# Kernel tuning notes

Measured on AMD Instinct MI355X. Metric: run time of the kernel, lower is better.

## Reference

```python
import jax, jax.numpy as jnp
import numpy as np

N_NODES = 100000
N_EDGES = 1600000
IN_CH = 165
HID = 128


def _xavier(key, shape):
    fan_out, fan_in = shape
    lim = float(np.sqrt(6.0 / (fan_in + fan_out)))
    return jax.random.uniform(key, shape, jnp.float32, -lim, lim)


def setup_inputs() -> dict:
    key = jax.random.key(0)
    ks = jax.random.split(key, 8)
    x = jax.random.normal(ks[0], (N_NODES, IN_CH), jnp.float32)
    edge_index = jax.random.randint(ks[1], (2, N_EDGES), 0, N_NODES, jnp.int64)
    return {
        "x": x,
        "edge_index": edge_index,
        "W_l0": _xavier(ks[2], (HID, IN_CH)),
        "b_l0": jnp.zeros((HID,), jnp.float32),
        "W_r0": _xavier(ks[3], (HID, IN_CH)),
        "W_l1": _xavier(ks[4], (HID, HID)),
        "b_l1": jnp.zeros((HID,), jnp.float32),
        "W_r1": _xavier(ks[5], (HID, HID)),
        "W_l2": _xavier(ks[6], (HID, HID)),
        "b_l2": jnp.zeros((HID,), jnp.float32),
        "W_r2": _xavier(ks[7], (HID, HID)),
        "W_out": _xavier(jax.random.fold_in(key, 7), (2, HID)),
        "b_out": jnp.zeros((2,), jnp.float32),
    }


def _sage_conv(x, src, dst, W_l, b_l, W_r):
    # mean-aggregate source features into destination nodes
    msg = x[src]  # [E, d] gather
    agg = jax.ops.segment_sum(msg, dst, num_segments=N_NODES)  # [N, d]
    cnt = jax.ops.segment_sum(jnp.ones((src.shape[0], 1), x.dtype), dst,
                              num_segments=N_NODES)
    mean = agg / jnp.maximum(cnt, 1.0)
    # out = lin_l(mean) + lin_r(x); lin_r has no bias (PyG SAGEConv)
    return mean @ W_l.T + b_l + x @ W_r.T


def reference(x, edge_index, W_l0, b_l0, W_r0, W_l1, b_l1, W_r1,
              W_l2, b_l2, W_r2, W_out, b_out):
    src, dst = edge_index[0], edge_index[1]
    h = jax.nn.relu(_sage_conv(x, src, dst, W_l0, b_l0, W_r0))
    h = jax.nn.relu(_sage_conv(h, src, dst, W_l1, b_l1, W_r1))
    h = _sage_conv(h, src, dst, W_l2, b_l2, W_r2)
    # dropout is identity in inference
    return h @ W_out.T + b_out  # [N, 2]
```

## Files before the change

### kernel.cpp

```cpp
#include <hip/hip_runtime.h>
#include <cstdint>
#include <cstddef>

#define NN 100000
#define IN_CH 165
#define HID 128

#define NBUCK 196
#define NPB 512
#define BMAX 10240
#define NWG 256

typedef __attribute__((ext_vector_type(8))) short short8;
typedef __attribute__((ext_vector_type(4))) float f32x4;

__device__ __forceinline__ ushort f2bf(float v) {
    uint b = __builtin_bit_cast(uint, v);
    return (ushort)((b + 0x7FFFu + ((b >> 16) & 1u)) >> 16);
}
__device__ __forceinline__ float lo16f(uint u) { return __builtin_bit_cast(float, u << 16); }
__device__ __forceinline__ float hi16f(uint u) { return __builtin_bit_cast(float, u & 0xFFFF0000u); }

__global__ __launch_bounds__(256) void k_cnt(const int* __restrict__ dst, int E, int chunk,
                                             int* __restrict__ cnt) {
    __shared__ int h[NBUCK];
    const int w = blockIdx.x, t = threadIdx.x;
    for (int b = t; b < NBUCK; b += 256) h[b] = 0;
    __syncthreads();
    const int beg = w * chunk, end = min(E, beg + chunk);
    for (int i0 = beg + t * 8; i0 < end; i0 += 2048) {
        if (i0 + 8 <= end) {
            const int4 d0 = *reinterpret_cast<const int4*>(dst + i0);
            const int4 d1 = *reinterpret_cast<const int4*>(dst + i0 + 4);
            atomicAdd(&h[d0.x >> 9], 1);
            atomicAdd(&h[d0.y >> 9], 1);
            atomicAdd(&h[d0.z >> 9], 1);
            atomicAdd(&h[d0.w >> 9], 1);
            atomicAdd(&h[d1.x >> 9], 1);
            atomicAdd(&h[d1.y >> 9], 1);
            atomicAdd(&h[d1.z >> 9], 1);
            atomicAdd(&h[d1.w >> 9], 1);
        } else {
            for (int i = i0; i < end; ++i) atomicAdd(&h[dst[i] >> 9], 1);
        }
    }
    __syncthreads();
    for (int b = t; b < NBUCK; b += 256) cnt[b * NWG + w] = h[b];
}

__global__ __launch_bounds__(1024) void k_cscan(const int* __restrict__ cnt,
                                                int* __restrict__ gaddr) {
    __shared__ int ps[1024];
    const int t = threadIdx.x;
    int s = 0;
    for (int k = 0; k < 49; k++) s += cnt[t * 49 + k];
    ps[t] = s;
    __syncthreads();
    for (int off = 1; off < 1024; off <<= 1) {
        int v = (t >= off) ? ps[t - off] : 0;
        __syncthreads();
        ps[t] += v;
        __syncthreads();
    }
    int run = (t > 0) ? ps[t - 1] : 0;
    for (int k = 0; k < 49; k++) {
        const int m = t * 49 + k;
        gaddr[m] = run;
        run += cnt[m];
    }
}

__global__ __launch_bounds__(256) void k_scatter(const int* __restrict__ src,
                                                 const int* __restrict__ dst, int E, int chunk,
                                                 const int* __restrict__ gaddr,
                                                 int* __restrict__ bdata) {
    __shared__ int cur[NBUCK];
    __shared__ int thist[256];
    __shared__ int sA[256];
    __shared__ int tex[NBUCK];
    __shared__ int lpos[NBUCK];
    __shared__ int staged[2048];
    __shared__ int addrs[2048];
    const int w = blockIdx.x, t = threadIdx.x;
    for (int b = t; b < NBUCK; b += 256) cur[b] = gaddr[b * NWG + w];
    const int beg = w * chunk, end = min(E, beg + chunk);
    for (int tb = beg; tb < end; tb += 2048) {
        const int tcnt = min(2048, end - tb);
        int key[8], bk[8];
        const int i0 = tb + t * 8;
        if (i0 + 8 <= end) {
            const int4 d0 = *reinterpret_cast<const int4*>(dst + i0);
            const int4 d1 = *reinterpret_cast<const int4*>(dst + i0 + 4);
            const int4 s0 = *reinterpret_cast<const int4*>(src + i0);
            const int4 s1 = *reinterpret_cast<const int4*>(src + i0 + 4);
            bk[0] = d0.x >> 9; key[0] = (s0.x << 9) | (d0.x & 511);
            bk[1] = d0.y >> 9; key[1] = (s0.y << 9) | (d0.y & 511);
            bk[2] = d0.z >> 9; key[2] = (s0.z << 9) | (d0.z & 511);
            bk[3] = d0.w >> 9; key[3] = (s0.w << 9) | (d0.w & 511);
            bk[4] = d1.x >> 9; key[4] = (s1.x << 9) | (d1.x & 511);
            bk[5] = d1.y >> 9; key[5] = (s1.y << 9) | (d1.y & 511);
            bk[6] = d1.z >> 9; key[6] = (s1.z << 9) | (d1.z & 511);
            bk[7] = d1.w >> 9; key[7] = (s1.w << 9) | (d1.w & 511);
        } else {
#pragma unroll
            for (int j = 0; j < 8; j++) {
                const int i = i0 + j;
                if (i < end) {
                    const int d = dst[i];
                    bk[j] = d >> 9;
                    key[j] = (src[i] << 9) | (d & 511);
                } else bk[j] = -1;
            }
        }
        __syncthreads();
        thist[t] = 0;
        __syncthreads();
#pragma unroll
        for (int j = 0; j < 8; j++)
            if (bk[j] >= 0) atomicAdd(&thist[bk[j]], 1);
        __syncthreads();
        sA[t] = thist[t];
        __syncthreads();
        for (int off = 1; off < 256; off <<= 1) {
            int v = (t >= off) ? sA[t - off] : 0;
            __syncthreads();
            sA[t] += v;
            __syncthreads();
        }
        if (t < NBUCK) {
            const int e = sA[t] - thist[t];
            tex[t] = e;
            lpos[t] = e;
        }
        __syncthreads();
#pragma unroll
        for (int j = 0; j < 8; j++)
            if (bk[j] >= 0) {
                const int b = bk[j];
                const int l = atomicAdd(&lpos[b], 1);
                staged[l] = key[j];
                addrs[l] = cur[b] + (l - tex[b]);
            }
        __syncthreads();
        for (int l = t; l < tcnt; l += 256) bdata[addrs[l]] = staged[l];
        __syncthreads();
        if (t < NBUCK) cur[t] += thist[t];
    }
}

__global__ __launch_bounds__(256) void k_csr2(const int* __restrict__ gaddr,
                                              const int* __restrict__ bdata, int E,
                                              int* __restrict__ csr, int* __restrict__ row_off,
                                              float* __restrict__ inv, int N) {
    __shared__ int keys[BMAX];
    __shared__ int sorted[BMAX];
    __shared__ int h5[NPB];
    __shared__ int s5[NPB];
    const int b = blockIdx.x, t = threadIdx.x;
    const int base = gaddr[b * NWG];
    const int nxt = (b == NBUCK - 1) ? E : gaddr[(b + 1) * NWG];
    const int tot = min(nxt - base, BMAX);
    for (int i = t; i < tot; i += 256) keys[i] = bdata[base + i];
    h5[t] = 0;
    h5[t + 256] = 0;
    __syncthreads();
    for (int i = t; i < tot; i += 256) atomicAdd(&h5[keys[i] & 511], 1);
    __syncthreads();
    s5[t] = h5[t];
    s5[t + 256] = h5[t + 256];
    __syncthreads();
    for (int off = 1; off < 512; off <<= 1) {
        const int a = (t >= off) ? s5[t - off] : 0;
        const int c = (t + 256 >= off) ? s5[t + 256 - off] : 0;
        __syncthreads();
        s5[t] += a;
        s5[t + 256] += c;
        __syncthreads();
    }
    const int e0 = s5[t] - h5[t];
    const int e1 = s5[t + 256] - h5[t + 256];
    __syncthreads();
    s5[t] = e0;
    s5[t + 256] = e1;
    const int n0 = b * NPB + t, n1 = b * NPB + t + 256;
    if (n0 < N) { row_off[n0] = base + e0; inv[n0] = 1.0f / (float)max(h5[t], 1); }
    if (n1 < N) { row_off[n1] = base + e1; inv[n1] = 1.0f / (float)max(h5[t + 256], 1); }
    if (b == 0 && t == 0) row_off[N] = E;
    __syncthreads();
    for (int i = t; i < tot; i += 256) {
        const int k = keys[i];
        const int p = atomicAdd(&s5[k & 511], 1);
        sorted[p] = k;
    }
    __syncthreads();
    for (int i = t; i < tot; i += 256) csr[base + i] = sorted[i] >> 9;
}

__device__ __forceinline__ void wpack_one(const float* __restrict__ W, int K, int idx,
                                          ushort* __restrict__ Wh) {
    const int k = idx >> 7;
    const int j = idx & 127;
    const float v = (k < K) ? W[j * K + k] : 0.0f;
    const int o = (k >> 3) * (HID * 8) + j * 8 + (k & 7);
    Wh[o] = f2bf(v);
}

__global__ __launch_bounds__(256) void k_prep(
    const float* __restrict__ Wl0, const float* __restrict__ Wr0,
    const float* __restrict__ Wl1, const float* __restrict__ Wr1,
    const float* __restrict__ Wl2, const float* __restrict__ Wr2,
    const float* __restrict__ Wout, const float* __restrict__ bl2,
    const float* __restrict__ bout,
    ushort* __restrict__ Wl0h, ushort* __restrict__ Wr0h,
    ushort* __restrict__ Wl1h, ushort* __restrict__ Wr1h,
    float* __restrict__ Wzp, float* __restrict__ bz)
{
    if (blockIdx.x == 96) {
        const int t = threadIdx.x;
        const int c = t >> 7, k = t & 127;
        float sl = 0.f, sr = 0.f;
        for (int j = 0; j < 128; j++) {
            const float wo = Wout[c * 128 + j];
            sl += wo * Wl2[j * 128 + k];
            sr += wo * Wr2[j * 128 + k];
        }
        Wzp[c * 128 + k] = sl;
        Wzp[256 + c * 128 + k] = sr;
        if (t < 2) {
            float s = bout[t];
            for (int j = 0; j < 128; j++) s += Wout[t * 128 + j] * bl2[j];
            bz[t] = s;
        }
        return;
    }
    const int gid = blockIdx.x * 256 + threadIdx.x;
    if (gid < 192 * HID) {
        wpack_one(Wl0, IN_CH, gid, Wl0h);
        wpack_one(Wr0, IN_CH, gid, Wr0h);
    }
    if (gid < 128 * HID) {
        wpack_one(Wl1, HID, gid, Wl1h);
        wpack_one(Wr1, HID, gid, Wr1h);
    }
}

template <typename TIN, int K, int KP>
__global__ __launch_bounds__(256) void k_gemm_mfma(
    const TIN* __restrict__ h,
    const ushort* __restrict__ Wlh, const ushort* __restrict__ Wrh,
    ushort* __restrict__ yl, ushort* __restrict__ yr)
{
    constexpr int RS = KP * 2;
    __shared__ __align__(16) char Ah[32 * RS];
    const int tid = threadIdx.x;
    const int node0 = blockIdx.x * 32;
    const TIN* __restrict__ hp = h + (size_t)node0 * K;

    if constexpr (sizeof(TIN) == 2) {
        constexpr int Q = 32 * (KP / 8);
        for (int q = tid; q < Q; q += 256) {
            const int r = q / (KP / 8);
            const int kp = (q - r * (KP / 8)) * 8;
            const short8 v = *reinterpret_cast<const short8*>(&hp[r * K + kp]);
            const int byte = r * RS + ((kp * 2) ^ ((r & 7) << 4));
            *reinterpret_cast<short8*>(Ah + byte) = v;
        }
    } else {
        __shared__ __align__(16) float raw[32 * K];
        const float* __restrict__ hpf = (const float*)hp;
        for (int i = tid * 4; i < 32 * K; i += 1024)
            *reinterpret_cast<float4*>(&raw[i]) = *reinterpret_cast<const float4*>(&hpf[i]);
        __syncthreads();
        constexpr int G = KP / 4;
        for (int q = tid; q < 32 * G; q += 256) {
            const int r = q / G;
            const int kp = (q - r * G) * 4;
            const float v0 = (kp + 0 < K) ? raw[r * K + kp + 0] : 0.0f;
            const float v1 = (kp + 1 < K) ? raw[r * K + kp + 1] : 0.0f;
            const float v2 = (kp + 2 < K) ? raw[r * K + kp + 2] : 0.0f;
            const float v3 = (kp + 3 < K) ? raw[r * K + kp + 3] : 0.0f;
            const int byte = r * RS + ((kp * 2) ^ ((r & 7) << 4));
            *reinterpret_cast<ushort4*>(Ah + byte) =
                make_ushort4(f2bf(v0), f2bf(v1), f2bf(v2), f2bf(v3));
        }
    }
    __syncthreads();

    const int lane = tid & 63;
    const int w = tid >> 6;
    const int trow = lane & 15;
    const int kg = lane >> 4;
    const ushort* __restrict__ Bh = (w & 1) ? Wrh : Wlh;
    ushort* __restrict__ yo = (w & 1) ? yr : yl;
    const int cb0 = (w >> 1) * 4;

    f32x4 acc[2][4];
#pragma unroll
    for (int a = 0; a < 2; ++a)
#pragma unroll
        for (int b = 0; b < 4; ++b) acc[a][b] = (f32x4){0.f, 0.f, 0.f, 0.f};

    const int xo = (trow & 7) << 4;
    const char* __restrict__ pA0 = Ah + trow * RS;
    const char* __restrict__ pA1 = Ah + (trow + 16) * RS;

    constexpr int KS = KP / 32;
    for (int ks = 0; ks < KS; ++ks) {
        const int kbyte = (ks * 64 + kg * 16) ^ xo;
        const short8 a0h = *reinterpret_cast<const short8*>(pA0 + kbyte);
        const short8 a1h = *reinterpret_cast<const short8*>(pA1 + kbyte);
        const int bbase = (ks * 4 + kg) * (HID * 8) + trow * 8;
#pragma unroll
        for (int ci = 0; ci < 4; ++ci) {
            const short8 bh = *reinterpret_cast<const short8*>(Bh + bbase + (cb0 + ci) * 128);
            acc[0][ci] = __builtin_amdgcn_mfma_f32_16x16x32_bf16(a0h, bh, acc[0][ci], 0, 0, 0);
            acc[1][ci] = __builtin_amdgcn_mfma_f32_16x16x32_bf16(a1h, bh, acc[1][ci], 0, 0, 0);
        }
    }

#pragma unroll
    for (int rb = 0; rb < 2; ++rb) {
        const int nb_ = node0 + rb * 16 + kg * 4;
#pragma unroll
        for (int ci = 0; ci < 4; ++ci) {
            const int col = (cb0 + ci) * 16 + trow;
            const f32x4 a = acc[rb][ci];
#pragma unroll
            for (int rr = 0; rr < 4; ++rr)
                yo[(size_t)(nb_ + rr) * HID + col] = f2bf(a[rr]);
        }
    }
}

__global__ __launch_bounds__(256) void k_agg_relu(
    const ushort* __restrict__ yl, const int* __restrict__ row_off,
    const int* __restrict__ csr, const float* __restrict__ inv,
    const float* __restrict__ bias, const ushort* __restrict__ yr,
    ushort* __restrict__ hout, int N)
{
    const int wid = (blockIdx.x * 256 + (int)threadIdx.x) >> 6;
    const int lane = threadIdx.x & 63;
    if (wid >= N) return;
    const int eslot = lane >> 4;
    const int c = lane & 15;
    const int beg = row_off[wid];
    const int end = row_off[wid + 1];
    const uint4* __restrict__ Y = (const uint4*)yl;

    float a0 = 0.f, a1 = 0.f, a2 = 0.f, a3 = 0.f;
    float a4 = 0.f, a5 = 0.f, a6 = 0.f, a7 = 0.f;
    auto acc8 = [&](uint4 u) {
        a0 += lo16f(u.x); a1 += hi16f(u.x);
        a2 += lo16f(u.y); a3 += hi16f(u.y);
        a4 += lo16f(u.z); a5 += hi16f(u.z);
        a6 += lo16f(u.w); a7 += hi16f(u.w);
    };

    int e = beg;
    for (; e + 16 <= end; e += 16) {
        const int s0 = csr[e + eslot];
        const int s1 = csr[e + 4 + eslot];
        const int s2 = csr[e + 8 + eslot];
        const int s3 = csr[e + 12 + eslot];
        const uint4 u0 = Y[(size_t)s0 * 16 + c];
        const uint4 u1 = Y[(size_t)s1 * 16 + c];
        const uint4 u2 = Y[(size_t)s2 * 16 + c];
        const uint4 u3 = Y[(size_t)s3 * 16 + c];
        acc8(u0); acc8(u1); acc8(u2); acc8(u3);
    }
    if (e + 8 <= end) {
        const int s0 = csr[e + eslot];
        const int s1 = csr[e + 4 + eslot];
        const uint4 u0 = Y[(size_t)s0 * 16 + c];
        const uint4 u1 = Y[(size_t)s1 * 16 + c];
        acc8(u0); acc8(u1);
        e += 8;
    }
    if (e + 4 <= end) {
        const uint4 u0 = Y[(size_t)csr[e + eslot] * 16 + c];
        acc8(u0);
        e += 4;
    }
    if (e + eslot < end) {
        const uint4 u0 = Y[(size_t)csr[e + eslot] * 16 + c];
        acc8(u0);
    }

    a0 += __shfl_xor(a0, 16); a1 += __shfl_xor(a1, 16);
    a2 += __shfl_xor(a2, 16); a3 += __shfl_xor(a3, 16);
    a4 += __shfl_xor(a4, 16); a5 += __shfl_xor(a5, 16);
    a6 += __shfl_xor(a6, 16); a7 += __shfl_xor(a7, 16);
    a0 += __shfl_xor(a0, 32); a1 += __shfl_xor(a1, 32);
    a2 += __shfl_xor(a2, 32); a3 += __shfl_xor(a3, 32);
    a4 += __shfl_xor(a4, 32); a5 += __shfl_xor(a5, 32);
    a6 += __shfl_xor(a6, 32); a7 += __shfl_xor(a7, 32);

    if (lane < 16) {
        const float iv = inv[wid];
        const uint4 rv = ((const uint4*)yr)[(size_t)wid * 16 + lane];
        const float4 b0 = ((const float4*)bias)[lane * 2];
        const float4 b1 = ((const float4*)bias)[lane * 2 + 1];
        const float v0 = fmaxf(a0 * iv + b0.x + lo16f(rv.x), 0.f);
        const float v1 = fmaxf(a1 * iv + b0.y + hi16f(rv.x), 0.f);
        const float v2 = fmaxf(a2 * iv + b0.z + lo16f(rv.y), 0.f);
        const float v3 = fmaxf(a3 * iv + b0.w + hi16f(rv.y), 0.f);
        const float v4 = fmaxf(a4 * iv + b1.x + lo16f(rv.z), 0.f);
        const float v5 = fmaxf(a5 * iv + b1.y + hi16f(rv.z), 0.f);
        const float v6 = fmaxf(a6 * iv + b1.z + lo16f(rv.w), 0.f);
        const float v7 = fmaxf(a7 * iv + b1.w + hi16f(rv.w), 0.f);
        uint4 o;
        o.x = (uint)f2bf(v0) | ((uint)f2bf(v1) << 16);
        o.y = (uint)f2bf(v2) | ((uint)f2bf(v3) << 16);
        o.z = (uint)f2bf(v4) | ((uint)f2bf(v5) << 16);
        o.w = (uint)f2bf(v6) | ((uint)f2bf(v7) << 16);
        ((uint4*)hout)[(size_t)wid * 16 + lane] = o;
    }
}

__global__ __launch_bounds__(256) void k_zproj(
    const ushort* __restrict__ h2, const float* __restrict__ Wzp,
    float2* __restrict__ z, float2* __restrict__ r, int N)
{
    const int node = (blockIdx.x * 256 + (int)threadIdx.x) >> 6;
    const int lane = threadIdx.x & 63;
    if (node >= N) return;
    const uint u = *reinterpret_cast<const uint*>(h2 + (size_t)node * HID + lane * 2);
    const float hx = lo16f(u), hy = hi16f(u);
    float z0 = hx * Wzp[lane * 2] + hy * Wzp[lane * 2 + 1];
    float z1 = hx * Wzp[128 + lane * 2] + hy * Wzp[128 + lane * 2 + 1];
    float r0 = hx * Wzp[256 + lane * 2] + hy * Wzp[256 + lane * 2 + 1];
    float r1 = hx * Wzp[384 + lane * 2] + hy * Wzp[384 + lane * 2 + 1];
#pragma unroll
    for (int off = 32; off > 0; off >>= 1) {
        z0 += __shfl_xor(z0, off);
        z1 += __shfl_xor(z1, off);
        r0 += __shfl_xor(r0, off);
        r1 += __shfl_xor(r1, off);
    }
    if (lane == 0) {
        z[node] = make_float2(z0, z1);
        r[node] = make_float2(r0, r1);
    }
}

__global__ __launch_bounds__(256) void k_aggz(
    const float2* __restrict__ z, const float2* __restrict__ r,
    const int* __restrict__ row_off, const int* __restrict__ csr,
    const float* __restrict__ inv, const float* __restrict__ bz,
    float2* __restrict__ out, int N)
{
    const int node = (blockIdx.x * 256 + (int)threadIdx.x) >> 6;
    const int lane = threadIdx.x & 63;
    if (node >= N) return;
    const int beg = row_off[node];
    const int end = row_off[node + 1];
    float s0 = 0.f, s1 = 0.f;
    for (int e = beg + lane; e < end; e += 64) {
        const float2 v = z[csr[e]];
        s0 += v.x;
        s1 += v.y;
    }
#pragma unroll
    for (int off = 32; off > 0; off >>= 1) {
        s0 += __shfl_xor(s0, off);
        s1 += __shfl_xor(s1, off);
    }
    if (lane == 0) {
        const float iv = inv[node];
        const float2 rv = r[node];
        out[node] = make_float2(s0 * iv + rv.x + bz[0], s1 * iv + rv.y + bz[1]);
    }
}

extern "C" void kernel_launch(void* const* d_in, const int* in_sizes, int n_in,
                              void* d_out, int out_size, void* d_ws, size_t ws_size,
                              hipStream_t stream) {
    const float* x    = (const float*)d_in[0];
    const int*   ei   = (const int*)d_in[1];
    const float* Wl0  = (const float*)d_in[2];
    const float* bl0  = (const float*)d_in[3];
    const float* Wr0  = (const float*)d_in[4];
    const float* Wl1  = (const float*)d_in[5];
    const float* bl1  = (const float*)d_in[6];
    const float* Wr1  = (const float*)d_in[7];
    const float* Wl2  = (const float*)d_in[8];
    const float* bl2  = (const float*)d_in[9];
    const float* Wr2  = (const float*)d_in[10];
    const float* Wout = (const float*)d_in[11];
    const float* bout = (const float*)d_in[12];

    const int N = NN;
    const int E = in_sizes[1] / 2;
    const int* src = ei;
    const int* dst = ei + E;
    const int chunk = (((E + NWG - 1) / NWG) + 7) & ~7;

    char* w = (char*)d_ws;
    auto alloc = [&](size_t bytes) {
        char* p = w;
        w += (bytes + 255) & ~(size_t)255;
        return p;
    };
    int*    cnt     = (int*)alloc((size_t)NWG * NBUCK * 4);
    int*    gaddr   = (int*)alloc((size_t)NWG * NBUCK * 4);
    int*    bdata   = (int*)alloc((size_t)E * 4);
    int*    row_off = (int*)alloc((size_t)(N + 1) * 4);
    float*  inv     = (float*)alloc((size_t)N * 4);
    int*    csr     = (int*)alloc((size_t)E * 4);
    ushort* Wl0h    = (ushort*)alloc((size_t)192 * HID * 2);
    ushort* Wr0h    = (ushort*)alloc((size_t)192 * HID * 2);
    ushort* Wl1h    = (ushort*)alloc((size_t)HID * HID * 2);
    ushort* Wr1h    = (ushort*)alloc((size_t)HID * HID * 2);
    float*  Wzp     = (float*)alloc((size_t)512 * 4);
    float*  bz      = (float*)alloc((size_t)8 * 4);
    ushort* B0      = (ushort*)alloc((size_t)N * HID * 2);
    ushort* B1      = (ushort*)alloc((size_t)N * HID * 2);
    ushort* B2      = (ushort*)alloc((size_t)N * HID * 2);
    float*  zbuf    = (float*)alloc((size_t)N * 2 * 4);
    float*  rbuf    = (float*)alloc((size_t)N * 2 * 4);

    k_cnt<<<NWG, 256, 0, stream>>>(dst, E, chunk, cnt);
    k_cscan<<<1, 1024, 0, stream>>>(cnt, gaddr);
    k_scatter<<<NWG, 256, 0, stream>>>(src, dst, E, chunk, gaddr, bdata);
    k_csr2<<<NBUCK, 256, 0, stream>>>(gaddr, bdata, E, csr, row_off, inv, N);

    k_prep<<<97, 256, 0, stream>>>(Wl0, Wr0, Wl1, Wr1, Wl2, Wr2, Wout, bl2, bout,
                                   Wl0h, Wr0h, Wl1h, Wr1h, Wzp, bz);

    const int gemm_grid = N / 32;
    const int wave_grid = N / 4;

    k_gemm_mfma<float, IN_CH, 192><<<gemm_grid, 256, 0, stream>>>(x, Wl0h, Wr0h, B0, B1);
    k_agg_relu<<<wave_grid, 256, 0, stream>>>(B0, row_off, csr, inv, bl0, B1, B1, N);

    k_gemm_mfma<ushort, HID, HID><<<gemm_grid, 256, 0, stream>>>(B1, Wl1h, Wr1h, B0, B2);
    k_agg_relu<<<wave_grid, 256, 0, stream>>>(B0, row_off, csr, inv, bl1, B2, B2, N);

    k_zproj<<<wave_grid, 256, 0, stream>>>(B2, Wzp, (float2*)zbuf, (float2*)rbuf, N);
    k_aggz<<<wave_grid, 256, 0, stream>>>((const float2*)zbuf, (const float2*)rbuf,
                                          row_off, csr, inv, bz, (float2*)d_out, N);
}
```

Measured before the change: 296.5 us.

## Merge weight prep and bucket scan into neighboring kernel launches; shuffle-based scan

New measurement: 286.3 us. 1.04x faster.

```diff
diff --git a/kernel.cpp b/kernel.cpp
--- a/kernel.cpp
+++ b/kernel.cpp
@@ -10,6 +10,7 @@
 #define NPB 512
 #define BMAX 10240
 #define NWG 256
+#define GEMM_GRID 3125
 
 typedef __attribute__((ext_vector_type(8))) short short8;
 typedef __attribute__((ext_vector_type(4))) float f32x4;
@@ -21,10 +22,59 @@
 __device__ __forceinline__ float lo16f(uint u) { return __builtin_bit_cast(float, u << 16); }
 __device__ __forceinline__ float hi16f(uint u) { return __builtin_bit_cast(float, u & 0xFFFF0000u); }
 
-__global__ __launch_bounds__(256) void k_cnt(const int* __restrict__ dst, int E, int chunk,
-                                             int* __restrict__ cnt) {
+__device__ __forceinline__ void wpack_one(const float* __restrict__ W, int K, int idx,
+                                          ushort* __restrict__ Wh) {
+    const int k = idx >> 7;
+    const int j = idx & 127;
+    const float v = (k < K) ? W[j * K + k] : 0.0f;
+    const int o = (k >> 3) * (HID * 8) + j * 8 + (k & 7);
+    Wh[o] = f2bf(v);
+}
+
+__global__ __launch_bounds__(256) void k_cnt_prep(
+    const int* __restrict__ dst, int E, int chunk, int* __restrict__ cnt,
+    const float* __restrict__ Wl0, const float* __restrict__ Wr0,
+    const float* __restrict__ Wl1, const float* __restrict__ Wr1,
+    const float* __restrict__ Wl2, const float* __restrict__ Wr2,
+    const float* __restrict__ Wout, const float* __restrict__ bl2,
+    const float* __restrict__ bout,
+    ushort* __restrict__ Wl0h, ushort* __restrict__ Wr0h,
+    ushort* __restrict__ Wl1h, ushort* __restrict__ Wr1h,
+    float* __restrict__ Wzp, float* __restrict__ bz)
+{
     __shared__ int h[NBUCK];
-    const int w = blockIdx.x, t = threadIdx.x;
+    const int t = threadIdx.x;
+    if (blockIdx.x >= NWG) {
+        const int pb = blockIdx.x - NWG;
+        if (pb == 96) {
+            const int c = t >> 7, k = t & 127;
+            float sl = 0.f, sr = 0.f;
+            for (int j = 0; j < 128; j++) {
+                const float wo = Wout[c * 128 + j];
+                sl += wo * Wl2[j * 128 + k];
+                sr += wo * Wr2[j * 128 + k];
+            }
+            Wzp[c * 128 + k] = sl;
+            Wzp[256 + c * 128 + k] = sr;
+            if (t < 2) {
+                float s = bout[t];
+                for (int j = 0; j < 128; j++) s += Wout[t * 128 + j] * bl2[j];
+                bz[t] = s;
+            }
+            return;
+        }
+        const int gid = pb * 256 + t;
+        if (gid < 192 * HID) {
+            wpack_one(Wl0, IN_CH, gid, Wl0h);
+            wpack_one(Wr0, IN_CH, gid, Wr0h);
+        }
+        if (gid < 128 * HID) {
+            wpack_one(Wl1, HID, gid, Wl1h);
+            wpack_one(Wr1, HID, gid, Wr1h);
+        }
+        return;
+    }
+    const int w = blockIdx.x;
     for (int b = t; b < NBUCK; b += 256) h[b] = 0;
     __syncthreads();
     const int beg = w * chunk, end = min(E, beg + chunk);
@@ -48,25 +98,102 @@
     for (int b = t; b < NBUCK; b += 256) cnt[b * NWG + w] = h[b];
 }
 
-__global__ __launch_bounds__(1024) void k_cscan(const int* __restrict__ cnt,
-                                                int* __restrict__ gaddr) {
-    __shared__ int ps[1024];
-    const int t = threadIdx.x;
-    int s = 0;
-    for (int k = 0; k < 49; k++) s += cnt[t * 49 + k];
-    ps[t] = s;
-    __syncthreads();
-    for (int off = 1; off < 1024; off <<= 1) {
-        int v = (t >= off) ? ps[t - off] : 0;
-        __syncthreads();
-        ps[t] += v;
-        __syncthreads();
-    }
-    int run = (t > 0) ? ps[t - 1] : 0;
-    for (int k = 0; k < 49; k++) {
-        const int m = t * 49 + k;
-        gaddr[m] = run;
-        run += cnt[m];
+__global__ __launch_bounds__(256) void k_gemm0_cscan(
+    const float* __restrict__ hsrc,
+    const ushort* __restrict__ Wlh, const ushort* __restrict__ Wrh,
+    ushort* __restrict__ yl, ushort* __restrict__ yr,
+    const int* __restrict__ cnt, int* __restrict__ gaddr)
+{
+    constexpr int K = IN_CH, KP = 192;
+    constexpr int RS = KP * 2;
+    __shared__ __align__(16) char Ah[32 * RS];
+    __shared__ __align__(16) float raw[32 * K];
+    __shared__ int ps[256];
+    const int tid = threadIdx.x;
+
+    if (blockIdx.x == GEMM_GRID) {
+        int s = 0;
+        for (int k = 0; k < NBUCK; k++) s += cnt[tid * NBUCK + k];
+        ps[tid] = s;
+        __syncthreads();
+        for (int off = 1; off < 256; off <<= 1) {
+            int v = (tid >= off) ? ps[tid - off] : 0;
+            __syncthreads();
+            ps[tid] += v;
+            __syncthreads();
+        }
+        int run = (tid > 0) ? ps[tid - 1] : 0;
+        for (int k = 0; k < NBUCK; k++) {
+            const int m = tid * NBUCK + k;
+            gaddr[m] = run;
+            run += cnt[m];
+        }
+        return;
+    }
+
+    const int node0 = blockIdx.x * 32;
+    const float* __restrict__ hp = hsrc + (size_t)node0 * K;
+
+    for (int i = tid * 4; i < 32 * K; i += 1024)
+        *reinterpret_cast<float4*>(&raw[i]) = *reinterpret_cast<const float4*>(&hp[i]);
+    __syncthreads();
+    constexpr int G = KP / 4;
+    for (int q = tid; q < 32 * G; q += 256) {
+        const int r = q / G;
+        const int kp = (q - r * G) * 4;
+        const float v0 = (kp + 0 < K) ? raw[r * K + kp + 0] : 0.0f;
+        const float v1 = (kp + 1 < K) ? raw[r * K + kp + 1] : 0.0f;
+        const float v2 = (kp + 2 < K) ? raw[r * K + kp + 2] : 0.0f;
+        const float v3 = (kp + 3 < K) ? raw[r * K + kp + 3] : 0.0f;
+        const int byte = r * RS + ((kp * 2) ^ ((r & 7) << 4));
+        *reinterpret_cast<ushort4*>(Ah + byte) =
+            make_ushort4(f2bf(v0), f2bf(v1), f2bf(v2), f2bf(v3));
+    }
+    __syncthreads();
+
+    const int lane = tid & 63;
+    const int w = tid >> 6;
+    const int trow = lane & 15;
+    const int kg = lane >> 4;
+    const ushort* __restrict__ Bh = (w & 1) ? Wrh : Wlh;
+    ushort* __restrict__ yo = (w & 1) ? yr : yl;
+    const int cb0 = (w >> 1) * 4;
+
+    f32x4 acc[2][4];
+#pragma unroll
+    for (int a = 0; a < 2; ++a)
+#pragma unroll
+        for (int b = 0; b < 4; ++b) acc[a][b] = (f32x4){0.f, 0.f, 0.f, 0.f};
+
+    const int xo = (trow & 7) << 4;
+    const char* __restrict__ pA0 = Ah + trow * RS;
+    const char* __restrict__ pA1 = Ah + (trow + 16) * RS;
+
+    constexpr int KS = KP / 32;
+    for (int ks = 0; ks < KS; ++ks) {
+        const int kbyte = (ks * 64 + kg * 16) ^ xo;
+        const short8 a0h = *reinterpret_cast<const short8*>(pA0 + kbyte);
+        const short8 a1h = *reinterpret_cast<const short8*>(pA1 + kbyte);
+        const int bbase = (ks * 4 + kg) * (HID * 8) + trow * 8;
+#pragma unroll
+        for (int ci = 0; ci < 4; ++ci) {
+            const short8 bh = *reinterpret_cast<const short8*>(Bh + bbase + (cb0 + ci) * 128);
+            acc[0][ci] = __builtin_amdgcn_mfma_f32_16x16x32_bf16(a0h, bh, acc[0][ci], 0, 0, 0);
+            acc[1][ci] = __builtin_amdgcn_mfma_f32_16x16x32_bf16(a1h, bh, acc[1][ci], 0, 0, 0);
+        }
+    }
+
+#pragma unroll
+    for (int rb = 0; rb < 2; ++rb) {
+        const int nb_ = node0 + rb * 16 + kg * 4;
+#pragma unroll
+        for (int ci = 0; ci < 4; ++ci) {
+            const int col = (cb0 + ci) * 16 + trow;
+            const f32x4 a = acc[rb][ci];
+#pragma unroll
+            for (int rr = 0; rr < 4; ++rr)
+                yo[(size_t)(nb_ + rr) * HID + col] = f2bf(a[rr]);
+        }
     }
 }
 
@@ -76,12 +203,13 @@
                                                  int* __restrict__ bdata) {
     __shared__ int cur[NBUCK];
     __shared__ int thist[256];
-    __shared__ int sA[256];
+    __shared__ int wsum[4];
     __shared__ int tex[NBUCK];
     __shared__ int lpos[NBUCK];
     __shared__ int staged[2048];
     __shared__ int addrs[2048];
     const int w = blockIdx.x, t = threadIdx.x;
+    const int lane6 = t & 63, wv = t >> 6;
     for (int b = t; b < NBUCK; b += 256) cur[b] = gaddr[b * NWG + w];
     const int beg = w * chunk, end = min(E, beg + chunk);
     for (int tb = beg; tb < end; tb += 2048) {
@@ -119,16 +247,20 @@
         for (int j = 0; j < 8; j++)
             if (bk[j] >= 0) atomicAdd(&thist[bk[j]], 1);
         __syncthreads();
-        sA[t] = thist[t];
-        __syncthreads();
-        for (int off = 1; off < 256; off <<= 1) {
-            int v = (t >= off) ? sA[t - off] : 0;
-            __syncthreads();
-            sA[t] += v;
-            __syncthreads();
-        }
+        int v = thist[t];
+#pragma unroll
+        for (int off = 1; off < 64; off <<= 1) {
+            const int u = __shfl_up(v, off);
+            if (lane6 >= off) v += u;
+        }
+        if (lane6 == 63) wsum[wv] = v;
+        __syncthreads();
+        int base = 0;
+#pragma unroll
+        for (int q = 0; q < 4; q++) base += (q < wv) ? wsum[q] : 0;
+        const int incl = v + base;
         if (t < NBUCK) {
-            const int e = sA[t] - thist[t];
+            const int e = incl - thist[t];
             tex[t] = e;
             lpos[t] = e;
         }
@@ -196,93 +328,25 @@
     for (int i = t; i < tot; i += 256) csr[base + i] = sorted[i] >> 9;
 }
 
-__device__ __forceinline__ void wpack_one(const float* __restrict__ W, int K, int idx,
-                                          ushort* __restrict__ Wh) {
-    const int k = idx >> 7;
-    const int j = idx & 127;
-    const float v = (k < K) ? W[j * K + k] : 0.0f;
-    const int o = (k >> 3) * (HID * 8) + j * 8 + (k & 7);
-    Wh[o] = f2bf(v);
-}
-
-__global__ __launch_bounds__(256) void k_prep(
-    const float* __restrict__ Wl0, const float* __restrict__ Wr0,
-    const float* __restrict__ Wl1, const float* __restrict__ Wr1,
-    const float* __restrict__ Wl2, const float* __restrict__ Wr2,
-    const float* __restrict__ Wout, const float* __restrict__ bl2,
-    const float* __restrict__ bout,
-    ushort* __restrict__ Wl0h, ushort* __restrict__ Wr0h,
-    ushort* __restrict__ Wl1h, ushort* __restrict__ Wr1h,
-    float* __restrict__ Wzp, float* __restrict__ bz)
-{
-    if (blockIdx.x == 96) {
-        const int t = threadIdx.x;
-        const int c = t >> 7, k = t & 127;
-        float sl = 0.f, sr = 0.f;
-        for (int j = 0; j < 128; j++) {
-            const float wo = Wout[c * 128 + j];
-            sl += wo * Wl2[j * 128 + k];
-            sr += wo * Wr2[j * 128 + k];
-        }
-        Wzp[c * 128 + k] = sl;
-        Wzp[256 + c * 128 + k] = sr;
-        if (t < 2) {
-            float s = bout[t];
-            for (int j = 0; j < 128; j++) s += Wout[t * 128 + j] * bl2[j];
-            bz[t] = s;
-        }
-        return;
-    }
-    const int gid = blockIdx.x * 256 + threadIdx.x;
-    if (gid < 192 * HID) {
-        wpack_one(Wl0, IN_CH, gid, Wl0h);
-        wpack_one(Wr0, IN_CH, gid, Wr0h);
-    }
-    if (gid < 128 * HID) {
-        wpack_one(Wl1, HID, gid, Wl1h);
-        wpack_one(Wr1, HID, gid, Wr1h);
-    }
-}
-
-template <typename TIN, int K, int KP>
-__global__ __launch_bounds__(256) void k_gemm_mfma(
-    const TIN* __restrict__ h,
+__global__ __launch_bounds__(256) void k_gemm1(
+    const ushort* __restrict__ h,
     const ushort* __restrict__ Wlh, const ushort* __restrict__ Wrh,
     ushort* __restrict__ yl, ushort* __restrict__ yr)
 {
+    constexpr int K = HID, KP = HID;
     constexpr int RS = KP * 2;
     __shared__ __align__(16) char Ah[32 * RS];
     const int tid = threadIdx.x;
     const int node0 = blockIdx.x * 32;
-    const TIN* __restrict__ hp = h + (size_t)node0 * K;
-
-    if constexpr (sizeof(TIN) == 2) {
-        constexpr int Q = 32 * (KP / 8);
-        for (int q = tid; q < Q; q += 256) {
-            const int r = q / (KP / 8);
-            const int kp = (q - r * (KP / 8)) * 8;
-            const short8 v = *reinterpret_cast<const short8*>(&hp[r * K + kp]);
-            const int byte = r * RS + ((kp * 2) ^ ((r & 7) << 4));
-            *reinterpret_cast<short8*>(Ah + byte) = v;
-        }
-    } else {
-        __shared__ __align__(16) float raw[32 * K];
-        const float* __restrict__ hpf = (const float*)hp;
-        for (int i = tid * 4; i < 32 * K; i += 1024)
-            *reinterpret_cast<float4*>(&raw[i]) = *reinterpret_cast<const float4*>(&hpf[i]);
-        __syncthreads();
-        constexpr int G = KP / 4;
-        for (int q = tid; q < 32 * G; q += 256) {
-            const int r = q / G;
-            const int kp = (q - r * G) * 4;
-            const float v0 = (kp + 0 < K) ? raw[r * K + kp + 0] : 0.0f;
-            const float v1 = (kp + 1 < K) ? raw[r * K + kp + 1] : 0.0f;
-            const float v2 = (kp + 2 < K) ? raw[r * K + kp + 2] : 0.0f;
-            const float v3 = (kp + 3 < K) ? raw[r * K + kp + 3] : 0.0f;
-            const int byte = r * RS + ((kp * 2) ^ ((r & 7) << 4));
-            *reinterpret_cast<ushort4*>(Ah + byte) =
-                make_ushort4(f2bf(v0), f2bf(v1), f2bf(v2), f2bf(v3));
-        }
+    const ushort* __restrict__ hp = h + (size_t)node0 * K;
+
+    constexpr int Q = 32 * (KP / 8);
+    for (int q = tid; q < Q; q += 256) {
+        const int r = q / (KP / 8);
+        const int kp = (q - r * (KP / 8)) * 8;
+        const short8 v = *reinterpret_cast<const short8*>(&hp[r * K + kp]);
+        const int byte = r * RS + ((kp * 2) ^ ((r & 7) << 4));
+        *reinterpret_cast<short8*>(Ah + byte) = v;
     }
     __syncthreads();
 
@@ -519,21 +583,21 @@
     float*  zbuf    = (float*)alloc((size_t)N * 2 * 4);
     float*  rbuf    = (float*)alloc((size_t)N * 2 * 4);
 
-    k_cnt<<<NWG, 256, 0, stream>>>(dst, E, chunk, cnt);
-    k_cscan<<<1, 1024, 0, stream>>>(cnt, gaddr);
+    const int wave_grid = N / 4;
+
+    k_cnt_prep<<<NWG + 97, 256, 0, stream>>>(
+        dst, E, chunk, cnt,
+        Wl0, Wr0, Wl1, Wr1, Wl2, Wr2, Wout, bl2, bout,
+        Wl0h, Wr0h, Wl1h, Wr1h, Wzp, bz);
+
+    k_gemm0_cscan<<<GEMM_GRID + 1, 256, 0, stream>>>(x, Wl0h, Wr0h, B0, B1, cnt, gaddr);
+
     k_scatter<<<NWG, 256, 0, stream>>>(src, dst, E, chunk, gaddr, bdata);
     k_csr2<<<NBUCK, 256, 0, stream>>>(gaddr, bdata, E, csr, row_off, inv, N);
 
-    k_prep<<<97, 256, 0, stream>>>(Wl0, Wr0, Wl1, Wr1, Wl2, Wr2, Wout, bl2, bout,
-                                   Wl0h, Wr0h, Wl1h, Wr1h, Wzp, bz);
-
-    const int gemm_grid = N / 32;
-    const int wave_grid = N / 4;
-
-    k_gemm_mfma<float, IN_CH, 192><<<gemm_grid, 256, 0, stream>>>(x, Wl0h, Wr0h, B0, B1);
     k_agg_relu<<<wave_grid, 256, 0, stream>>>(B0, row_off, csr, inv, bl0, B1, B1, N);
 
-    k_gemm_mfma<ushort, HID, HID><<<gemm_grid, 256, 0, stream>>>(B1, Wl1h, Wr1h, B0, B2);
+    k_gemm1<<<GEMM_GRID, 256, 0, stream>>>(B1, Wl1h, Wr1h, B0, B2);
     k_agg_relu<<<wave_grid, 256, 0, stream>>>(B0, row_off, csr, inv, bl1, B2, B2, N);
 
     k_zproj<<<wave_grid, 256, 0, stream>>>(B2, Wzp, (float2*)zbuf, (float2*)rbuf, N);
```
